# Kernel tuning notes

Hardware: AMD Instinct MI355X
Metric: run time of the kernel (lower is better)

Reference implementation:

```python
import jax, jax.numpy as jnp
import numpy as np

N_NODES = 100_000
N_EDGES = 1_600_000
D_FEAT = 128
D_HID = 128
D_OUT = 1


def _w(key, fan_in, fan_out):
    # PyG Linear default (glorot-ish); exact init irrelevant for a math reference
    return jax.random.normal(key, (fan_in, fan_out), dtype=jnp.float32) * (1.0 / np.sqrt(fan_in))


def setup_inputs() -> dict:
    key = jax.random.key(0)
    ks = jax.random.split(key, 20)
    inp = {
        "x": jax.random.normal(ks[0], (N_NODES, D_FEAT), dtype=jnp.float32),
        "edge_index": jax.random.randint(ks[1], (2, N_EDGES), 0, N_NODES, dtype=jnp.int32),
    }
    dims = [(D_FEAT, D_HID), (D_HID, D_HID), (D_HID, D_OUT)]
    i = 2
    for li, (din, dout) in enumerate(dims, start=1):
        inp[f"Wk{li}"] = _w(ks[i + 0], din, dout)
        inp[f"Wq{li}"] = _w(ks[i + 1], din, dout)
        inp[f"Wv{li}"] = _w(ks[i + 2], din, dout)
        inp[f"Ws{li}"] = _w(ks[i + 3], din, dout)
        inp[f"b{li}"] = jnp.zeros((dout,), dtype=jnp.float32)
        i += 4
    return inp


def _res_gated_conv(x, src, dst, Wk, Wq, Wv, Ws, b):
    # out_i = Ws x_i + b + sum_{j->i} sigmoid(Wk x_i + Wq x_j) * (Wv x_j)
    k = x @ Wk          # [N, Dout] (keyed by target)
    q = x @ Wq          # [N, Dout] (keyed by source)
    v = x @ Wv          # [N, Dout]
    eta = jax.nn.sigmoid(k[dst] + q[src])          # [E, Dout] edge gate
    msg = eta * v[src]                             # [E, Dout]
    agg = jax.ops.segment_sum(msg, dst, num_segments=x.shape[0])  # scatter-add
    return agg + x @ Ws + b


def reference(x, edge_index, Wk1, Wq1, Wv1, Ws1, b1, Wk2, Wq2, Wv2, Ws2, b2,
              Wk3, Wq3, Wv3, Ws3, b3):
    src = edge_index[0]
    dst = edge_index[1]
    x = jax.nn.relu(_res_gated_conv(x, src, dst, Wk1, Wq1, Wv1, Ws1, b1))
    x = jax.nn.relu(_res_gated_conv(x, src, dst, Wk2, Wq2, Wv2, Ws2, b2))
    return _res_gated_conv(x, src, dst, Wk3, Wq3, Wv3, Ws3, b3)  # [N, 1]
```

## Files before the change

### kernel.cpp

```cpp
#include <hip/hip_runtime.h>
#include <hip/hip_bf16.h>
#include <cstdint>

typedef unsigned short u16;
typedef unsigned int   u32;
typedef __attribute__((ext_vector_type(8))) short bf16x8;
typedef __attribute__((ext_vector_type(4))) float f32x4;

#define NEG_LOG2E -1.44269504088896f

__device__ __forceinline__ float bf2f(u16 u) {
    union { u32 i; float f; } c; c.i = ((u32)u) << 16; return c.f;
}
__device__ __forceinline__ u16 f2bf(float f) {
    union { float f; u32 i; } c; c.f = f;
    u32 x = c.i;
    return (u16)((x + 0x7fffu + ((x >> 16) & 1u)) >> 16);
}
__device__ __forceinline__ void bfu2(u32 p, float& lo, float& hi) {
    union { u32 i; float f; } a, b;
    a.i = p << 16; b.i = p & 0xffff0000u;
    lo = a.f; hi = b.f;
}
__device__ __forceinline__ float gate(float zt) {
    return __builtin_amdgcn_rcpf(1.0f + __builtin_amdgcn_exp2f(zt));
}

#define CSR_CH 2048
#define XS 136

struct P8 { const float* p[8]; };
__global__ __launch_bounds__(256)
void prep_hist_k(P8 wsrc, u16* __restrict__ Wt,
                 const int* __restrict__ dst, int* __restrict__ cnt,
                 int nE, int NA, int nbuck) {
    __shared__ int lh[512];
    int t = threadIdx.x;
    if (blockIdx.x < 64) {
        int mat = blockIdx.x >> 3, seg = blockIdx.x & 7;
        const float* W = wsrc.p[mat];
        u16* T = Wt + (size_t)mat * 16384;
        for (int p = 0; p < 8; ++p) {
            int idx = seg * 2048 + p * 256 + t;
            int k = idx >> 7, n = idx & 127;
            T[n * 128 + k] = f2bf(W[k * 128 + n]);
        }
    } else {
        int b = blockIdx.x - 64;
        for (int i = t; i < nbuck; i += 256) lh[i] = 0;
        __syncthreads();
        int i0 = b * CSR_CH, iend = min(i0 + CSR_CH, nE);
        for (int i = i0 + t; i < iend; i += 256) atomicAdd(&lh[dst[i] >> 8], 1);
        __syncthreads();
        for (int i = t; i < nbuck; i += 256) cnt[i * NA + b] = lh[i];
    }
}

__global__ __launch_bounds__(256)
void scan_part_k(const int* __restrict__ arr, int* __restrict__ part, int M) {
    __shared__ int wsum[4];
    int t = threadIdx.x, lane = t & 63, wave = t >> 6;
    int i0 = blockIdx.x * 1024 + t * 4;
    int s = 0;
    for (int j = 0; j < 4; ++j) { int i = i0 + j; if (i < M) s += arr[i]; }
    for (int off = 32; off > 0; off >>= 1) s += __shfl_xor(s, off);
    if (lane == 0) wsum[wave] = s;
    __syncthreads();
    if (t == 0) part[blockIdx.x] = wsum[0] + wsum[1] + wsum[2] + wsum[3];
}

__global__ __launch_bounds__(256)
void scan_emit2_k(const int* __restrict__ arr, const int* __restrict__ part,
                  int* __restrict__ outp, int M, int total, int nparts) {
    __shared__ int sh[512];
    __shared__ int woff[4];
    int t = threadIdx.x, lane = t & 63, wave = t >> 6;
    sh[t]       = (t < nparts)       ? part[t]       : 0;
    sh[t + 256] = (t + 256 < nparts) ? part[t + 256] : 0;
    __syncthreads();
    for (int off = 1; off < 512; off <<= 1) {
        int u0 = (t >= off)       ? sh[t - off]       : 0;
        int u1 = (t + 256 >= off) ? sh[t + 256 - off] : 0;
        __syncthreads();
        sh[t] += u0; sh[t + 256] += u1;
        __syncthreads();
    }
    int base = (blockIdx.x == 0) ? 0 : sh[blockIdx.x - 1];
    __syncthreads();

    int i0 = blockIdx.x * 1024 + t * 4;
    int d[4]; int s = 0;
    for (int j = 0; j < 4; ++j) { int i = i0 + j; d[j] = (i < M) ? arr[i] : 0; s += d[j]; }
    int ws = s;
    for (int off = 1; off < 64; off <<= 1) {
        int u = __shfl_up(ws, off);
        if (lane >= off) ws += u;
    }
    if (lane == 63) woff[wave] = ws;
    __syncthreads();
    for (int w = 0; w < wave; ++w) base += woff[w];
    int ex = base + ws - s;
    for (int j = 0; j < 4; ++j) {
        int i = i0 + j;
        if (i < M) outp[i] = ex;
        ex += d[j];
    }
    if (blockIdx.x == 0 && t == 0) outp[M] = total;
}

__global__ __launch_bounds__(256)
void sortA_scat(const int* __restrict__ src, const int* __restrict__ dst,
                const int* __restrict__ scnt, u32* __restrict__ tkey,
                int nE, int NA, int nbuck) {
    __shared__ int lh[512];
    __shared__ int lbase[512];
    int t = threadIdx.x, b = blockIdx.x;
    for (int i = t; i < nbuck; i += 256) { lh[i] = 0; lbase[i] = scnt[i * NA + b]; }
    __syncthreads();
    int i0 = b * CSR_CH, iend = min(i0 + CSR_CH, nE);
    for (int i = i0 + t; i < iend; i += 256) {
        int d = dst[i], s = src[i];
        int bk = d >> 8;
        int r = atomicAdd(&lh[bk], 1);
        tkey[lbase[bk] + r] = ((u32)(d & 255) << 24) | (u32)s;
    }
}

__device__ __forceinline__
void sortB_body(const u32* __restrict__ tkey, const int* __restrict__ scnt,
                int* __restrict__ rowp, int* __restrict__ ssrc,
                int NA, int N, int nE, int b, int* h, int* offv) {
    int t = threadIdx.x;
    int base = scnt[b * NA];
    int endp = scnt[(b + 1) * NA];
    h[t] = 0;
    __syncthreads();
    for (int i = base + t; i < endp; i += 256)
        atomicAdd(&h[tkey[i] >> 24], 1);
    __syncthreads();
    int v = h[t];
    offv[t] = v;
    __syncthreads();
    for (int d = 1; d < 256; d <<= 1) {
        int u = (t >= d) ? offv[t - d] : 0;
        __syncthreads();
        offv[t] += u;
        __syncthreads();
    }
    int ex = offv[t] - v;
    __syncthreads();
    offv[t] = ex;
    h[t] = 0;
    __syncthreads();
    int dglob = b * 256 + t;
    if (dglob < N) rowp[dglob] = base + ex;
    if (b == 0 && t == 0) rowp[N] = nE;
    for (int i = base + t; i < endp; i += 256) {
        u32 k = tkey[i];
        int loc = k >> 24;
        int r = atomicAdd(&h[loc], 1);
        ssrc[base + offv[loc] + r] = (int)(k & 0xFFFFFFu);
    }
}

template<int F32>
__device__ __forceinline__
void gemm_body(int bid, u16* xs, u16* wsl,
               const void* __restrict__ Xv, const u16* __restrict__ Wt,
               const float* __restrict__ bias,
               u16* __restrict__ KS, u16* __restrict__ QV, int nrows)
{
    const int tid  = threadIdx.x;
    const int wave = tid >> 6, lane = tid & 63;
    const int quad = lane >> 4, l16 = lane & 15;
    const int r0 = bid * 128;

    for (int p = 0; p < 8; ++p) {
        int c = p * 256 + tid;
        int row = c >> 4;
        int col = (c & 15) * 8;
        int gr = r0 + row; if (gr >= nrows) gr = nrows - 1;
        if (F32) {
            const float* sp = (const float*)Xv + (size_t)gr * 128 + col;
            float4 f0 = *(const float4*)(sp);
            float4 f1 = *(const float4*)(sp + 4);
            uint4 st;
            st.x = ((u32)f2bf(f0.y) << 16) | f2bf(f0.x);
            st.y = ((u32)f2bf(f0.w) << 16) | f2bf(f0.z);
            st.z = ((u32)f2bf(f1.y) << 16) | f2bf(f1.x);
            st.w = ((u32)f2bf(f1.w) << 16) | f2bf(f1.z);
            *(uint4*)(&xs[row * XS + col]) = st;
        } else {
            uint4 d = *(const uint4*)((const u16*)Xv + (size_t)gr * 128 + col);
            *(uint4*)(&xs[row * XS + col]) = d;
        }
    }

    for (int wi = 0; wi < 4; ++wi) {
        __syncthreads();
        const u16* Wsrc = Wt + wi * (128 * 128);
        for (int p = 0; p < 8; ++p) {
            int c = p * 256 + tid;
            int row = c >> 4;
            int col = (c & 15) * 8;
            uint4 d = *(const uint4*)(Wsrc + row * 128 + col);
            *(uint4*)(&wsl[row * XS + col]) = d;
        }
        __syncthreads();

        f32x4 acc[2][8];
        for (int mt = 0; mt < 2; ++mt)
            for (int nt = 0; nt < 8; ++nt) acc[mt][nt] = (f32x4)0.0f;

        const int cbase = wave * 32;
        for (int kt = 0; kt < 4; ++kt) {
            bf16x8 a0 = *(const bf16x8*)&wsl[(cbase + l16)      * XS + kt * 32 + quad * 8];
            bf16x8 a1 = *(const bf16x8*)&wsl[(cbase + 16 + l16) * XS + kt * 32 + quad * 8];
            for (int nt = 0; nt < 8; ++nt) {
                bf16x8 b = *(const bf16x8*)&xs[(nt * 16 + l16) * XS + kt * 32 + quad * 8];
                acc[0][nt] = __builtin_amdgcn_mfma_f32_16x16x32_bf16(a0, b, acc[0][nt], 0, 0, 0);
                acc[1][nt] = __builtin_amdgcn_mfma_f32_16x16x32_bf16(a1, b, acc[1][nt], 0, 0, 0);
            }
        }

        float4 bias4[2];
        if (wi == 3) {
            bias4[0] = *(const float4*)(bias + cbase + quad * 4);
            bias4[1] = *(const float4*)(bias + cbase + 16 + quad * 4);
        }
        for (int mt = 0; mt < 2; ++mt) {
            int chb = cbase + mt * 16 + quad * 4;
            for (int nt = 0; nt < 8; ++nt) {
                int node = r0 + nt * 16 + l16;
                if (node >= nrows) continue;
                f32x4 v = acc[mt][nt];
                float x0 = v[0], x1 = v[1], x2 = v[2], x3 = v[3];
                if (wi == 0 || wi == 1) {
                    x0 *= NEG_LOG2E; x1 *= NEG_LOG2E; x2 *= NEG_LOG2E; x3 *= NEG_LOG2E;
                } else if (wi == 3) {
                    x0 += bias4[mt].x; x1 += bias4[mt].y;
                    x2 += bias4[mt].z; x3 += bias4[mt].w;
                }
                uint2 st;
                st.x = ((u32)f2bf(x1) << 16) | f2bf(x0);
                st.y = ((u32)f2bf(x3) << 16) | f2bf(x2);
                size_t nb = (size_t)node * 256;
                if      (wi == 0) *(uint2*)(KS + nb + chb) = st;
                else if (wi == 3) *(uint2*)(KS + nb + 128 + chb) = st;
                else if (wi == 1) *(uint2*)(QV + nb + 2 * chb) = st;
                else              *(uint2*)(QV + nb + 2 * chb + 4) = st;
            }
        }
    }
}

__global__ __launch_bounds__(256, 2)
void sortB_gemm1(const u32* __restrict__ tkey, const int* __restrict__ scnt,
                 int* __restrict__ rowp, int* __restrict__ ssrc,
                 int NA, int N, int nE, int nbuck,
                 const float* __restrict__ x0, const u16* __restrict__ Wt,
                 const float* __restrict__ bias,
                 u16* __restrict__ KS, u16* __restrict__ QV)
{
    __shared__ u16 xs[128 * XS];
    __shared__ u16 wsl[128 * XS];
    if ((int)blockIdx.x < nbuck) {
        int* h = (int*)xs;
        int* offv = h + 256;
        sortB_body(tkey, scnt, rowp, ssrc, NA, N, nE, blockIdx.x, h, offv);
    } else {
        gemm_body<1>(blockIdx.x - nbuck, xs, wsl, x0, Wt, bias, KS, QV, N);
    }
}

__global__ __launch_bounds__(256, 2)
void gemm_l2(const u16* __restrict__ X, const u16* __restrict__ Wt,
             const float* __restrict__ bias,
             u16* __restrict__ KS, u16* __restrict__ QV, int nrows)
{
    __shared__ u16 xs[128 * XS];
    __shared__ u16 wsl[128 * XS];
    gemm_body<0>(blockIdx.x, xs, wsl, X, Wt, bias, KS, QV, nrows);
}

template<int MODE>
__global__ __launch_bounds__(256)
void edge_csr2(const int* __restrict__ rowp, const int* __restrict__ ssrc,
               const u16* __restrict__ KS, const u16* __restrict__ QV,
               u16* __restrict__ Xout,
               const float* __restrict__ Wk3, const float* __restrict__ Wq3,
               const float* __restrict__ Wv3, const float* __restrict__ Ws3,
               const float* __restrict__ b3,
               float* __restrict__ k3, float2* __restrict__ qv3,
               float* __restrict__ s3, int N)
{
    const int lane = threadIdx.x & 63;
    const int half = lane >> 5;
    const int t    = lane & 31;
    int gw = blockIdx.x * (blockDim.x >> 6) + (threadIdx.x >> 6);
    int nw = gridDim.x * (blockDim.x >> 6);

    float4 wk4, wq4, wv4, ws4;
    float bias3 = 0.0f;
    if (MODE == 1) {
        wk4 = *(const float4*)(Wk3 + 4 * t);
        wq4 = *(const float4*)(Wq3 + 4 * t);
        wv4 = *(const float4*)(Wv3 + 4 * t);
        ws4 = *(const float4*)(Ws3 + 4 * t);
        bias3 = b3[0];
    }

#define LOAD2(S0, S1) (*((const uint4*)(QV + (size_t)(half ? (S1) : (S0)) * 256) + t))
#define COMP(QVv, A0, A1, A2, A3)                                             \
    {                                                                         \
        float q0_, q1_, q2_, q3_, v0_, v1_, v2_, v3_;                         \
        bfu2((QVv).x, q0_, q1_); bfu2((QVv).y, q2_, q3_);                     \
        bfu2((QVv).z, v0_, v1_); bfu2((QVv).w, v2_, v3_);                     \
        A0 += gate(k0 + q0_) * v0_;  A1 += gate(k1 + q1_) * v1_;              \
        A2 += gate(k2 + q2_) * v2_;  A3 += gate(k3v + q3_) * v3_;             \
    }
#define LOADG(G, RA, RB)                                                      \
    {                                                                         \
        int s0_ = __builtin_amdgcn_readlane(sv, 4 * (G));                     \
        int s1_ = __builtin_amdgcn_readlane(sv, 4 * (G) + 1);                 \
        int s2_ = __builtin_amdgcn_readlane(sv, 4 * (G) + 2);                 \
        int s3_ = __builtin_amdgcn_readlane(sv, 4 * (G) + 3);                 \
        RA = LOAD2(s0_, s1_); RB = LOAD2(s2_, s3_);                           \
    }

    int d = gw;
    int begC = 0, endC = 0;
    if (d < N) { begC = rowp[d]; endC = rowp[d + 1]; }
    while (d < N) {
        int beg = begC, end = endC;
        int dn = d + nw;
        if (dn < N) { begC = rowp[dn]; endC = rowp[dn + 1]; }

        uint2 kk = *(const uint2*)(KS + (size_t)d * 256 + t * 4);
        uint2 ss = *(const uint2*)(KS + (size_t)d * 256 + 128 + t * 4);
        float k0, k1, k2, k3v;
        bfu2(kk.x, k0, k1); bfu2(kk.y, k2, k3v);
        float a0 = 0.f, a1 = 0.f, a2 = 0.f, a3 = 0.f;
        float e0 = 0.f, e1 = 0.f, e2 = 0.f, e3 = 0.f;

        for (int base = beg; base < end; base += 64) {
            int e = base + lane;
            int sv = (e < end) ? ssrc[e] : 0;
            int m = end - base; if (m > 64) m = 64;
            int ng = m >> 2;
            int j = ng << 2;
            if (ng > 0) {
                uint4 xA, xB, yA, yB;
                LOADG(0, xA, xB);
                int g = 1;
                for (; g + 1 < ng; g += 2) {
                    LOADG(g, yA, yB);
                    COMP(xA, a0, a1, a2, a3);
                    COMP(xB, e0, e1, e2, e3);
                    LOADG(g + 1, xA, xB);
                    COMP(yA, a0, a1, a2, a3);
                    COMP(yB, e0, e1, e2, e3);
                }
                if (g < ng) {
                    LOADG(g, yA, yB);
                    COMP(xA, a0, a1, a2, a3);
                    COMP(xB, e0, e1, e2, e3);
                    COMP(yA, a0, a1, a2, a3);
                    COMP(yB, e0, e1, e2, e3);
                } else {
                    COMP(xA, a0, a1, a2, a3);
                    COMP(xB, e0, e1, e2, e3);
                }
            }
            if (j + 2 <= m) {
                int s0 = __builtin_amdgcn_readlane(sv, j);
                int s1 = __builtin_amdgcn_readlane(sv, j + 1);
                uint4 qA = LOAD2(s0, s1);
                COMP(qA, a0, a1, a2, a3);
                j += 2;
            }
            if (j < m) {
                int s0i = __builtin_amdgcn_readlane(sv, j);
                uint4 qv_ = *((const uint4*)(QV + (size_t)s0i * 256) + t);
                float q0_, q1_, q2_, q3_, v0_, v1_, v2_, v3_;
                bfu2(qv_.x, q0_, q1_); bfu2(qv_.y, q2_, q3_);
                bfu2(qv_.z, v0_, v1_); bfu2(qv_.w, v2_, v3_);
                if (half == 0) {
                    a0 += gate(k0 + q0_) * v0_;  a1 += gate(k1 + q1_) * v1_;
                    a2 += gate(k2 + q2_) * v2_;  a3 += gate(k3v + q3_) * v3_;
                }
            }
        }
#undef LOADG
#undef LOAD2
#undef COMP

        a0 += e0; a1 += e1; a2 += e2; a3 += e3;
        a0 += __shfl_xor(a0, 32);
        a1 += __shfl_xor(a1, 32);
        a2 += __shfl_xor(a2, 32);
        a3 += __shfl_xor(a3, 32);

        float s0f, s1f, s2f, s3f;
        bfu2(ss.x, s0f, s1f); bfu2(ss.y, s2f, s3f);
        float r0 = fmaxf(s0f + a0, 0.f);
        float r1 = fmaxf(s1f + a1, 0.f);
        float r2 = fmaxf(s2f + a2, 0.f);
        float r3 = fmaxf(s3f + a3, 0.f);

        if (MODE == 0) {
            if (half == 0) {
                uint2 st;
                st.x = ((u32)f2bf(r1) << 16) | f2bf(r0);
                st.y = ((u32)f2bf(r3) << 16) | f2bf(r2);
                *(uint2*)(Xout + (size_t)d * 128 + t * 4) = st;
            }
        } else {
            float pk = r0 * wk4.x + r1 * wk4.y + r2 * wk4.z + r3 * wk4.w;
            float pq = r0 * wq4.x + r1 * wq4.y + r2 * wq4.z + r3 * wq4.w;
            float pv = r0 * wv4.x + r1 * wv4.y + r2 * wv4.z + r3 * wv4.w;
            float ps = r0 * ws4.x + r1 * ws4.y + r2 * ws4.z + r3 * ws4.w;
            for (int off = 1; off < 32; off <<= 1) {
                pk += __shfl_xor(pk, off);
                pq += __shfl_xor(pq, off);
                pv += __shfl_xor(pv, off);
                ps += __shfl_xor(ps, off);
            }
            if (lane == 0) {
                k3[d]  = NEG_LOG2E * pk;
                qv3[d] = make_float2(NEG_LOG2E * pq, pv);
                s3[d]  = ps + bias3;
            }
        }
        d = dn;
    }
}

__global__ __launch_bounds__(256)
void edge3_csr(const int* __restrict__ rowp, const int* __restrict__ ssrc,
               const float* __restrict__ k3, const float2* __restrict__ qv3,
               const float* __restrict__ s3, float* __restrict__ outp, int N)
{
    int lane = threadIdx.x & 63;
    int gw = blockIdx.x * (blockDim.x >> 6) + (threadIdx.x >> 6);
    int nw = gridDim.x * (blockDim.x >> 6);
    for (int d = gw; d < N; d += nw) {
        int beg = rowp[d], end = rowp[d + 1];
        float kd = k3[d];
        float sum = 0.0f;
        for (int e = beg + lane; e < end; e += 64) {
            float2 qv = qv3[ssrc[e]];
            sum += gate(kd + qv.x) * qv.y;
        }
        for (int off = 32; off > 0; off >>= 1) sum += __shfl_xor(sum, off);
        if (lane == 0) outp[d] = s3[d] + sum;
    }
}

extern "C" void kernel_launch(void* const* d_in, const int* in_sizes, int n_in,
                              void* d_out, int out_size, void* d_ws, size_t ws_size,
                              hipStream_t stream)
{
    const float* x0 = (const float*)d_in[0];
    const int*   ei = (const int*)d_in[1];
    const int    N  = in_sizes[0] / 128;
    const int    E  = in_sizes[1] / 2;
    const int* src = ei;
    const int* dst = ei + E;

    const int NBUCK = (N + 255) >> 8;
    const int NA    = (E + CSR_CH - 1) / CSR_CH;
    const int M     = NBUCK * NA;
    const int nparts = (M + 1023) / 1024;

    char* ws = (char*)d_ws;
    size_t off = 0;
    auto carve = [&](size_t bytes) { void* p = ws + off; off += (bytes + 255) & ~(size_t)255; return p; };
    u16*    Wt   = (u16*)carve((size_t)8 * 16384 * sizeof(u16));
    u16*    bufX = (u16*)carve((size_t)N * 128 * sizeof(u16));
    u16*    KS   = (u16*)carve((size_t)N * 256 * sizeof(u16));
    u16*    QV   = (u16*)carve((size_t)N * 256 * sizeof(u16));
    int*    ssrc = (int*)carve((size_t)E * sizeof(int));
    u32*    tkey = (u32*)carve((size_t)E * sizeof(u32));
    int*    rowp = (int*)carve((size_t)(N + 1) * sizeof(int));
    int*    cnt  = (int*)carve((size_t)M * sizeof(int));
    int*    scnt = (int*)carve((size_t)(M + 1) * sizeof(int));
    int*    part = (int*)carve((size_t)512 * sizeof(int));
    float*  k3   = (float*)carve((size_t)N * sizeof(float));
    float2* qv3  = (float2*)carve((size_t)N * sizeof(float2));
    float*  s3   = (float*)carve((size_t)N * sizeof(float));

    P8 wp;
    wp.p[0] = (const float*)d_in[2];  wp.p[1] = (const float*)d_in[3];
    wp.p[2] = (const float*)d_in[4];  wp.p[3] = (const float*)d_in[5];
    wp.p[4] = (const float*)d_in[7];  wp.p[5] = (const float*)d_in[8];
    wp.p[6] = (const float*)d_in[9];  wp.p[7] = (const float*)d_in[10];

    int gb = (N + 127) / 128;

    prep_hist_k<<<64 + NA, 256, 0, stream>>>(wp, Wt, dst, cnt, E, NA, NBUCK);
    scan_part_k<<<nparts, 256, 0, stream>>>(cnt, part, M);
    scan_emit2_k<<<nparts, 256, 0, stream>>>(cnt, part, scnt, M, E, nparts);
    sortA_scat<<<NA, 256, 0, stream>>>(src, dst, scnt, tkey, E, NA, NBUCK);
    sortB_gemm1<<<NBUCK + gb, 256, 0, stream>>>(tkey, scnt, rowp, ssrc, NA, N, E, NBUCK,
        x0, Wt, (const float*)d_in[6], KS, QV);
    edge_csr2<0><<<4096, 256, 0, stream>>>(rowp, ssrc, KS, QV, bufX,
        nullptr, nullptr, nullptr, nullptr, nullptr, nullptr, nullptr, nullptr, N);
    gemm_l2<<<gb, 256, 0, stream>>>(bufX, Wt + 4 * 16384, (const float*)d_in[11], KS, QV, N);
    edge_csr2<1><<<4096, 256, 0, stream>>>(rowp, ssrc, KS, QV, nullptr,
        (const float*)d_in[12], (const float*)d_in[13], (const float*)d_in[14],
        (const float*)d_in[15], (const float*)d_in[16],
        k3, qv3, s3, N);
    edge3_csr<<<2048, 256, 0, stream>>>(rowp, ssrc, k3, qv3, s3, (float*)d_out, N);
}
```

Measured before the change: 538.0 us.

## Prefetch next node's CSR indices, K/S row, and first gathers across iterations

The aggregation kernels now load the next destination node's row pointers, source indices, and K/S features during the current node's work. The aggregation kernel also issues the first group of Q/V gathers for the next node before the epilogue. K and S are interleaved per channel, so one 16-byte load per lane fetches both. The aim is to hide the dependent-load latency chain (rowp, then ssrc, then QV) between nodes, at the cost of more live registers and clamped index loads.

```diff
diff --git a/kernel.cpp b/kernel.cpp
--- a/kernel.cpp
+++ b/kernel.cpp
@@ -245,8 +245,8 @@
                 st.x = ((u32)f2bf(x1) << 16) | f2bf(x0);
                 st.y = ((u32)f2bf(x3) << 16) | f2bf(x2);
                 size_t nb = (size_t)node * 256;
-                if      (wi == 0) *(uint2*)(KS + nb + chb) = st;
-                else if (wi == 3) *(uint2*)(KS + nb + 128 + chb) = st;
+                if      (wi == 0) *(uint2*)(KS + nb + 2 * chb) = st;
+                else if (wi == 3) *(uint2*)(KS + nb + 2 * chb + 4) = st;
                 else if (wi == 1) *(uint2*)(QV + nb + 2 * chb) = st;
                 else              *(uint2*)(QV + nb + 2 * chb + 4) = st;
             }
@@ -319,50 +319,71 @@
         A0 += gate(k0 + q0_) * v0_;  A1 += gate(k1 + q1_) * v1_;              \
         A2 += gate(k2 + q2_) * v2_;  A3 += gate(k3v + q3_) * v3_;             \
     }
-#define LOADG(G, RA, RB)                                                      \
+#define LOADG(SVV, G, RA, RB)                                                 \
     {                                                                         \
-        int s0_ = __builtin_amdgcn_readlane(sv, 4 * (G));                     \
-        int s1_ = __builtin_amdgcn_readlane(sv, 4 * (G) + 1);                 \
-        int s2_ = __builtin_amdgcn_readlane(sv, 4 * (G) + 2);                 \
-        int s3_ = __builtin_amdgcn_readlane(sv, 4 * (G) + 3);                 \
+        int s0_ = __builtin_amdgcn_readlane(SVV, 4 * (G));                    \
+        int s1_ = __builtin_amdgcn_readlane(SVV, 4 * (G) + 1);                \
+        int s2_ = __builtin_amdgcn_readlane(SVV, 4 * (G) + 2);                \
+        int s3_ = __builtin_amdgcn_readlane(SVV, 4 * (G) + 3);                \
         RA = LOAD2(s0_, s1_); RB = LOAD2(s2_, s3_);                           \
     }
 
     int d = gw;
-    int begC = 0, endC = 0;
-    if (d < N) { begC = rowp[d]; endC = rowp[d + 1]; }
+    int beg = 0, end = 0, sv = 0;
+    uint4 ks; ks.x = ks.y = ks.z = ks.w = 0u;
+    if (d < N) {
+        beg = rowp[d]; end = rowp[d + 1];
+        int e  = beg + lane;
+        int ec = (end > beg) ? ((e < end) ? e : end - 1) : 0;
+        sv = ssrc[ec];
+        ks = *((const uint4*)KS + (size_t)d * 32 + t);
+    }
+    int havePF = 0;
+    uint4 pA, pB;
+    pA.x = pA.y = pA.z = pA.w = 0u;
+    pB = pA;
+
     while (d < N) {
-        int beg = begC, end = endC;
         int dn = d + nw;
-        if (dn < N) { begC = rowp[dn]; endC = rowp[dn + 1]; }
-
-        uint2 kk = *(const uint2*)(KS + (size_t)d * 256 + t * 4);
-        uint2 ss = *(const uint2*)(KS + (size_t)d * 256 + 128 + t * 4);
+        int begN = 0, endN = 0, svN = 0;
+        uint4 ksN; ksN.x = ksN.y = ksN.z = ksN.w = 0u;
+        if (dn < N) {
+            begN = rowp[dn]; endN = rowp[dn + 1];
+            int e  = begN + lane;
+            int ec = (endN > begN) ? ((e < endN) ? e : endN - 1) : 0;
+            svN = ssrc[ec];
+            ksN = *((const uint4*)KS + (size_t)dn * 32 + t);
+        }
+
         float k0, k1, k2, k3v;
-        bfu2(kk.x, k0, k1); bfu2(kk.y, k2, k3v);
+        bfu2(ks.x, k0, k1); bfu2(ks.y, k2, k3v);
         float a0 = 0.f, a1 = 0.f, a2 = 0.f, a3 = 0.f;
         float e0 = 0.f, e1 = 0.f, e2 = 0.f, e3 = 0.f;
 
         for (int base = beg; base < end; base += 64) {
-            int e = base + lane;
-            int sv = (e < end) ? ssrc[e] : 0;
+            if (base > beg) {
+                int e  = base + lane;
+                int ec = (e < end) ? e : end - 1;
+                sv = ssrc[ec];
+            }
             int m = end - base; if (m > 64) m = 64;
             int ng = m >> 2;
             int j = ng << 2;
             if (ng > 0) {
                 uint4 xA, xB, yA, yB;
-                LOADG(0, xA, xB);
+                if (havePF && base == beg) { xA = pA; xB = pB; }
+                else LOADG(sv, 0, xA, xB);
                 int g = 1;
                 for (; g + 1 < ng; g += 2) {
-                    LOADG(g, yA, yB);
+                    LOADG(sv, g, yA, yB);
                     COMP(xA, a0, a1, a2, a3);
                     COMP(xB, e0, e1, e2, e3);
-                    LOADG(g + 1, xA, xB);
+                    LOADG(sv, g + 1, xA, xB);
                     COMP(yA, a0, a1, a2, a3);
                     COMP(yB, e0, e1, e2, e3);
                 }
                 if (g < ng) {
-                    LOADG(g, yA, yB);
+                    LOADG(sv, g, yA, yB);
                     COMP(xA, a0, a1, a2, a3);
                     COMP(xB, e0, e1, e2, e3);
                     COMP(yA, a0, a1, a2, a3);
@@ -391,6 +412,20 @@
                 }
             }
         }
+
+        havePF = 0;
+        if (dn < N) {
+            int mN = endN - begN; if (mN > 64) mN = 64;
+            if ((mN >> 2) > 0) {
+                int s0_ = __builtin_amdgcn_readlane(svN, 0);
+                int s1_ = __builtin_amdgcn_readlane(svN, 1);
+                int s2_ = __builtin_amdgcn_readlane(svN, 2);
+                int s3_ = __builtin_amdgcn_readlane(svN, 3);
+                pA = LOAD2(s0_, s1_);
+                pB = LOAD2(s2_, s3_);
+                havePF = 1;
+            }
+        }
 #undef LOADG
 #undef LOAD2
 #undef COMP
@@ -402,7 +437,7 @@
         a3 += __shfl_xor(a3, 32);
 
         float s0f, s1f, s2f, s3f;
-        bfu2(ss.x, s0f, s1f); bfu2(ss.y, s2f, s3f);
+        bfu2(ks.z, s0f, s1f); bfu2(ks.w, s2f, s3f);
         float r0 = fmaxf(s0f + a0, 0.f);
         float r1 = fmaxf(s1f + a1, 0.f);
         float r2 = fmaxf(s2f + a2, 0.f);
@@ -432,7 +467,8 @@
                 s3[d]  = ps + bias3;
             }
         }
-        d = dn;
+
+        d = dn; beg = begN; end = endN; sv = svN; ks = ksN;
     }
 }
 
@@ -444,16 +480,43 @@
     int lane = threadIdx.x & 63;
     int gw = blockIdx.x * (blockDim.x >> 6) + (threadIdx.x >> 6);
     int nw = gridDim.x * (blockDim.x >> 6);
-    for (int d = gw; d < N; d += nw) {
-        int beg = rowp[d], end = rowp[d + 1];
-        float kd = k3[d];
+
+    int d = gw;
+    int beg = 0, end = 0, sv = 0;
+    float kd = 0.f, sd = 0.f;
+    if (d < N) {
+        beg = rowp[d]; end = rowp[d + 1];
+        int e  = beg + lane;
+        int ec = (end > beg) ? ((e < end) ? e : end - 1) : 0;
+        sv = ssrc[ec];
+        kd = k3[d]; sd = s3[d];
+    }
+    while (d < N) {
+        int dn = d + nw;
+        int begN = 0, endN = 0, svN = 0;
+        float kdN = 0.f, sdN = 0.f;
+        if (dn < N) {
+            begN = rowp[dn]; endN = rowp[dn + 1];
+            int e  = begN + lane;
+            int ec = (endN > begN) ? ((e < endN) ? e : endN - 1) : 0;
+            svN = ssrc[ec];
+            kdN = k3[dn]; sdN = s3[dn];
+        }
+
         float sum = 0.0f;
-        for (int e = beg + lane; e < end; e += 64) {
+        int m = end - beg;
+        if (lane < m) {
+            float2 qv = qv3[sv];
+            sum = gate(kd + qv.x) * qv.y;
+        }
+        for (int e = beg + 64 + lane; e < end; e += 64) {
             float2 qv = qv3[ssrc[e]];
             sum += gate(kd + qv.x) * qv.y;
         }
         for (int off = 32; off > 0; off >>= 1) sum += __shfl_xor(sum, off);
-        if (lane == 0) outp[d] = s3[d] + sum;
+        if (lane == 0) outp[d] = sd + sum;
+
+        d = dn; beg = begN; end = endN; sv = svN; kd = kdN; sd = sdN;
     }
 }
 
```

Result: no change. 544.2 us (+1.1%).
